# Performance work log

Hardware: AMD Instinct MI355X
Metric: run time of the kernel (lower is better)

## Reference

```python
import jax, jax.numpy as jnp
import numpy as np

INTERVAL = 8
HEADS = 4
DIM = 64


def grid_shuffle(x, I):
    # rearrange 'b c (h i) (w j) -> (b i j) c h w' : stride-I residue grouping
    B, C, H, W = x.shape
    h, w = H // I, W // I
    x = x.reshape(B, C, h, I, w, I).transpose(0, 3, 5, 1, 2, 4)
    return x.reshape(B * I * I, C, h, w)


def grid_unshuffle(x, I, B):
    Bp, C, h, w = x.shape
    x = x.reshape(B, I, I, C, h, w).transpose(0, 3, 4, 1, 5, 2)
    return x.reshape(B, C, h * I, w * I)


def conv1x1(x, w, b):
    return jnp.einsum('oc,bchw->bohw', w, x) + b[None, :, None, None]


def pos_bias(h, w, W1, b1, W2, b2):
    # dynamic RPE: MLP over normalized relative coordinates -> [heads, N, N]
    ch = jnp.arange(h)
    cw = jnp.arange(w)
    coords = jnp.stack(jnp.meshgrid(ch, cw, indexing='ij'), -1).reshape(-1, 2).astype(jnp.float32)
    denom = jnp.array([max(h - 1, 1), max(w - 1, 1)], dtype=jnp.float32)
    rel = (coords[:, None, :] - coords[None, :, :]) / denom  # [N,N,2]
    hid = jax.nn.relu(rel @ W1 + b1)
    bias = hid @ W2 + b2  # [N,N,heads]
    return bias.transpose(2, 0, 1)


def mask_attn(q2d, k2d, v2d, bias, pw, pb, heads, scale):
    Bp, C, h, w = q2d.shape
    N, d = h * w, C // heads

    def to_tok(t):  # [Bp,C,h,w] -> [Bp,heads,N,d]
        return t.reshape(Bp, heads, d, N).transpose(0, 1, 3, 2)

    q, k, v = to_tok(q2d), to_tok(k2d), to_tok(v2d)
    attn = jnp.einsum('bhnd,bhmd->bhnm', q * scale, k) + bias[None]
    attn = jax.nn.softmax(attn, axis=-1)
    out = jnp.einsum('bhnm,bhmd->bhnd', attn, v)
    out2d = out.transpose(0, 1, 3, 2).reshape(Bp, C, h, w)
    return conv1x1(out2d, pw, pb)


def setup_inputs() -> dict:
    key = jax.random.key(0)
    ks = jax.random.split(key, 14)
    pos_hidden = DIM // 4  # 16
    s = 0.02
    return {
        'x': jax.random.normal(ks[0], (2, DIM, 160, 160), jnp.float32),
        'qkv_w': jax.random.normal(ks[1], (3 * DIM, DIM), jnp.float32) * s,
        'qkv_b': jnp.zeros((3 * DIM,), jnp.float32),
        'grid_w': jax.random.normal(ks[2], (DIM, DIM), jnp.float32) * s,
        'grid_b': jnp.zeros((DIM,), jnp.float32),
        'pos_w1': jax.random.normal(ks[3], (2, pos_hidden), jnp.float32) * s,
        'pos_b1': jnp.zeros((pos_hidden,), jnp.float32),
        'pos_w2': jax.random.normal(ks[4], (pos_hidden, HEADS), jnp.float32) * s,
        'pos_b2': jnp.zeros((HEADS,), jnp.float32),
        'proj1_w': jax.random.normal(ks[5], (DIM, DIM), jnp.float32) * s,
        'proj1_b': jnp.zeros((DIM,), jnp.float32),
        'proj2_w': jax.random.normal(ks[6], (DIM, DIM), jnp.float32) * s,
        'proj2_b': jnp.zeros((DIM,), jnp.float32),
    }


def reference(x, qkv_w, qkv_b, grid_w, grid_b, pos_w1, pos_b1, pos_w2, pos_b2,
              proj1_w, proj1_b, proj2_w, proj2_b):
    I = INTERVAL
    scale = (DIM // HEADS) ** -0.5
    B, C, H, W = x.shape
    qkv = conv1x1(x, qkv_w, qkv_b)
    x_grid = conv1x1(grid_shuffle(x, I), grid_w, grid_b)
    qkv = grid_shuffle(qkv, I)
    bias = pos_bias(H // I, W // I, pos_w1, pos_b1, pos_w2, pos_b2)
    q, k, v = jnp.split(qkv, 3, axis=1)
    out = mask_attn(x_grid, k, v, bias, proj1_w, proj1_b, HEADS, scale)
    out = mask_attn(q, x_grid, out, bias, proj2_w, proj2_b, HEADS, scale)
    return grid_unshuffle(out, I, B)
```

## Files before the change

kernel.cpp:

```cpp
#include <hip/hip_runtime.h>
#include <hip/hip_bf16.h>


#define N_TOK 400
#define NP    416
#define BP    128

typedef short bf16x8 __attribute__((ext_vector_type(8)));
typedef float f32x16 __attribute__((ext_vector_type(16)));

__device__ inline ushort f2bf(float f) {
    __hip_bfloat16 h = __float2bfloat16(f);
    return *reinterpret_cast<ushort*>(&h);
}
__device__ inline float bf2f(ushort u) {
    union { uint i; float f; } v; v.i = (uint)u << 16; return v.f;
}
__device__ inline uint pk2(float a, float b) {
    return (uint)f2bf(a) | ((uint)f2bf(b) << 16);
}
__device__ inline bf16x8 ld16(const ushort* p) {
    union { uint4 q; bf16x8 v; } u;
    u.q = *reinterpret_cast<const uint4*>(p);
    return u.v;
}
__device__ inline float fast_exp2(float x) {
#if __has_builtin(__builtin_amdgcn_exp2f)
    return __builtin_amdgcn_exp2f(x);
#else
    return __expf(x * 0.6931471805599453f);
#endif
}
__device__ inline float fast_rcp(float x) {
#if __has_builtin(__builtin_amdgcn_rcpf)
    return __builtin_amdgcn_rcpf(x);
#else
    return 1.0f / x;
#endif
}

#define L2E 1.4426950408889634f
#define QK_PRESCALE 0.36067376022224085f

__global__ __launch_bounds__(256) void k_prep(
    const float* __restrict__ W1, const float* __restrict__ B1,
    const float* __restrict__ W2, const float* __restrict__ B2,
    const float* __restrict__ qkv_w, const float* __restrict__ qkv_b,
    const float* __restrict__ grid_w, const float* __restrict__ grid_b,
    const float* __restrict__ p1w, const float* __restrict__ p2w,
    float* __restrict__ biasF, ushort* __restrict__ Wc, float* __restrict__ Bc,
    ushort* __restrict__ Wp1, ushort* __restrict__ Wp2)
{
    int blk = blockIdx.x;
    if (blk < 2704) {
        int idx = blk * 256 + threadIdx.x;
        if (idx >= 692224) return;
        int r = idx & 15, lane = (idx >> 4) & 63;
        int tile = idx >> 10;
        int mt = tile % 13, rem = tile / 13, qt = rem % 13, h = rem / 13;
        int n = qt * 32 + (lane & 31);
        int m = mt * 32 + (r & 3) + 8 * (r >> 2) + 4 * (lane >> 5);
        float val = 0.0f;
        if (n < 400 && m < 400) {
            float r0 = (float)(n / 20 - m / 20) * (1.0f / 19.0f);
            float r1 = (float)(n % 20 - m % 20) * (1.0f / 19.0f);
            float o = B2[h];
#pragma unroll
            for (int k = 0; k < 16; ++k) {
                float hh = r0 * W1[k] + r1 * W1[16 + k] + B1[k];
                hh = fmaxf(hh, 0.0f);
                o += hh * W2[k * 4 + h];
            }
            val = o * L2E;
        }
        biasF[idx] = val;
    } else {
        int t = (blk - 2704) * 256 + threadIdx.x;
        if (t < 16384) {
            int oc = t >> 6, k = t & 63;
            float v = (oc < 192) ? qkv_w[oc * 64 + k] : grid_w[(oc - 192) * 64 + k];
            Wc[t] = f2bf(v);
        } else if (t < 16384 + 4096) {
            Wp1[t - 16384] = f2bf(p1w[t - 16384]);
        } else if (t < 16384 + 8192) {
            Wp2[t - 16384 - 4096] = f2bf(p2w[t - 16384 - 4096]);
        } else if (t < 16384 + 8192 + 256) {
            int oc = t - 16384 - 8192;
            Bc[oc] = (oc < 192) ? qkv_b[oc] : grid_b[oc - 192];
        }
    }
}

__global__ __launch_bounds__(256) void k_conv(
    const float* __restrict__ x, const ushort* __restrict__ Wc,
    const float* __restrict__ Bc,
    ushort* __restrict__ Qb, ushort* __restrict__ Kb,
    ushort* __restrict__ Vb, ushort* __restrict__ XGb)
{
    __shared__ __align__(16) ushort XL[32 * 64];
    int blk = blockIdx.x;
    int b = blk / 800, rem = blk % 800;
    int H0 = rem / 5, wt = rem % 5;
    int w0 = wt * 32;
    int tid = threadIdx.x;

    {
        int c = tid >> 2, q4 = tid & 3;
        const float* xr = x + ((size_t)(b * 64 + c) * 160 + H0) * 160 + w0 + q4 * 8;
        float4 f0 = *reinterpret_cast<const float4*>(xr);
        float4 f1 = *reinterpret_cast<const float4*>(xr + 4);
        char* base = reinterpret_cast<char*>(XL);
#pragma unroll
        for (int k = 0; k < 8; ++k) {
            float v = (k < 4) ? ((const float*)&f0)[k] : ((const float*)&f1)[k - 4];
            int p = q4 * 8 + k;
            int byt = p * 128 + ((2 * c) ^ ((p & 7) << 4));
            *reinterpret_cast<ushort*>(base + byt) = f2bf(v);
        }
    }

    int lane = tid & 63, w = tid >> 6;
    int l31 = lane & 31, hi = lane >> 5;

    bf16x8 wf[2][4];
#pragma unroll
    for (int nt = 0; nt < 2; ++nt)
#pragma unroll
        for (int kk = 0; kk < 4; ++kk)
            wf[nt][kk] = ld16(&Wc[(size_t)(w * 64 + nt * 32 + l31) * 64 + kk * 16 + hi * 8]);
    __syncthreads();

    f32x16 acc0 = 0.0f, acc1 = 0.0f;
    const char* base = reinterpret_cast<const char*>(XL);
#pragma unroll
    for (int kk = 0; kk < 4; ++kk) {
        int byt = l31 * 128 + (((kk * 32 + hi * 16)) ^ ((l31 & 7) << 4));
        bf16x8 xf;
        {
            union { uint4 q; bf16x8 v; } u;
            u.q = *reinterpret_cast<const uint4*>(base + byt);
            xf = u.v;
        }
        acc0 = __builtin_amdgcn_mfma_f32_32x32x16_bf16(wf[0][kk], xf, acc0, 0, 0, 0);
        acc1 = __builtin_amdgcn_mfma_f32_32x32x16_bf16(wf[1][kk], xf, acc1, 0, 0, 0);
    }

    int W0 = w0 + l31, ww = W0 >> 3, j = W0 & 7;
    int bp = b * 64 + (H0 & 7) * 8 + j;
    int n  = (H0 >> 3) * 20 + ww;
    ushort* outb = (w == 0) ? Qb : (w == 1) ? Kb : (w == 2) ? Vb : XGb;
    float mul = (w <= 1) ? QK_PRESCALE : 1.0f;
    ushort* dst = outb + ((size_t)bp * NP + n) * 64;
#pragma unroll
    for (int nt = 0; nt < 2; ++nt) {
        const f32x16& a = nt ? acc1 : acc0;
#pragma unroll
        for (int g = 0; g < 4; ++g) {
            int cc = nt * 32 + 8 * g + 4 * hi;
            int oc = w * 64 + cc;
            uint2 uu;
            uu.x = pk2((a[4 * g + 0] + Bc[oc + 0]) * mul, (a[4 * g + 1] + Bc[oc + 1]) * mul);
            uu.y = pk2((a[4 * g + 2] + Bc[oc + 2]) * mul, (a[4 * g + 3] + Bc[oc + 3]) * mul);
            *reinterpret_cast<uint2*>(dst + cc) = uu;
        }
    }
}

__global__ __launch_bounds__(512, 4) void k_attn_mfma(
    const ushort* __restrict__ Qg, const ushort* __restrict__ Kg,
    const ushort* __restrict__ Vg, const float* __restrict__ biasF,
    ushort* __restrict__ O)
{
    __shared__ ushort Ks[NP * 16];
    __shared__ ushort Vt[16 * 424];
    int blk = blockIdx.x;
    int bp = blk >> 2, h = blk & 3;
    int tid = threadIdx.x;

    const ushort* Ksrc = Kg + (size_t)bp * NP * 64 + h * 16;
#pragma unroll
    for (int it = 0; it < 2; ++it) {
        int i = tid + it * 512;
        if (i < NP * 2) {
            int row = i >> 1, half = i & 1;
            *reinterpret_cast<uint4*>(&Ks[row * 16 + half * 8]) =
                *reinterpret_cast<const uint4*>(&Ksrc[(size_t)row * 64 + half * 8]);
        }
    }
    const ushort* Vsrc = Vg + (size_t)bp * NP * 64 + h * 16;
#pragma unroll
    for (int it = 0; it < 2; ++it) {
        int i = tid + it * 512;
        if (i < 800) {
            int row = i >> 1, hf = i & 1;
            uint4 v = *reinterpret_cast<const uint4*>(&Vsrc[(size_t)row * 64 + hf * 8]);
            const ushort* pv = reinterpret_cast<const ushort*>(&v);
#pragma unroll
            for (int k = 0; k < 8; ++k)
                Vt[(hf * 8 + k) * 424 + row] = pv[k];
        }
    }
    __syncthreads();

    int lane = tid & 63, w = tid >> 6;
    int l31 = lane & 31, hi = lane >> 5;
    const uint ONE2 = 0x3F803F80u;

    for (int qt = w; qt < 13; qt += 8) {
        int qbase = qt * 32;
        bf16x8 qf = ld16(&Qg[((size_t)bp * NP + qbase + l31) * 64 + h * 16 + hi * 8]);
        f32x16 acc = 0.0f;
        const f32x16* bfr = reinterpret_cast<const f32x16*>(
            biasF + ((size_t)(h * 169 + qt * 13)) * 1024 + lane * 16);

        f32x16 cb = bfr[0];

#pragma unroll
        for (int mt = 0; mt < 13; ++mt) {
            const int mbase = mt * 32;
            f32x16 nb;
            if (mt < 12) nb = bfr[mt + 1];

            __builtin_amdgcn_s_setprio(1);
            bf16x8 kf = ld16(&Ks[(mbase + l31) * 16 + hi * 8]);
            f32x16 sv = __builtin_amdgcn_mfma_f32_32x32x16_bf16(kf, qf, cb, 0, 0, 0);

            const int nv = (mt == 12) ? 8 : 16;
            float p[16];
#pragma unroll
            for (int r = 0; r < 16; ++r)
                if (r < nv) p[r] = fast_exp2(sv[r]);

            {
                uint c4 = pk2(p[0], p[1]), c5 = pk2(p[2], p[3]);
                uint c6 = pk2(p[4], p[5]), c7 = pk2(p[6], p[7]);
                asm("v_permlane32_swap_b32 %0, %1" : "+v"(c4), "+v"(c6));
                asm("v_permlane32_swap_b32 %0, %1" : "+v"(c5), "+v"(c7));
                union { uint u[4]; bf16x8 v; } A;
                A.u[0] = c4; A.u[1] = c5; A.u[2] = c6; A.u[3] = c7;
                bf16x8 vf;
                if (l31 < 16) vf = ld16(&Vt[l31 * 424 + mbase + hi * 8]);
                else { union { uint u[4]; bf16x8 v; } o; o.u[0]=o.u[1]=o.u[2]=o.u[3]=ONE2; vf = o.v; }
                acc = __builtin_amdgcn_mfma_f32_32x32x16_bf16(A.v, vf, acc, 0, 0, 0);
            }
            if (mt < 12) {
                uint c4 = pk2(p[8], p[9]),  c5 = pk2(p[10], p[11]);
                uint c6 = pk2(p[12], p[13]), c7 = pk2(p[14], p[15]);
                asm("v_permlane32_swap_b32 %0, %1" : "+v"(c4), "+v"(c6));
                asm("v_permlane32_swap_b32 %0, %1" : "+v"(c5), "+v"(c7));
                union { uint u[4]; bf16x8 v; } A;
                A.u[0] = c4; A.u[1] = c5; A.u[2] = c6; A.u[3] = c7;
                bf16x8 vf;
                if (l31 < 16) vf = ld16(&Vt[l31 * 424 + mbase + 16 + hi * 8]);
                else { union { uint u[4]; bf16x8 v; } o; o.u[0]=o.u[1]=o.u[2]=o.u[3]=ONE2; vf = o.v; }
                acc = __builtin_amdgcn_mfma_f32_32x32x16_bf16(A.v, vf, acc, 0, 0, 0);
            }
            __builtin_amdgcn_s_setprio(0);
            cb = nb;
        }

#pragma unroll
        for (int r = 0; r < 16; ++r) {
            int moff = (r & 3) + 8 * (r >> 2) + 4 * hi;
            int q = qbase + moff;
            float s = __shfl(acc[r], lane | 16);
            if (l31 < 16 && q < N_TOK)
                O[((size_t)bp * 400 + q) * 64 + h * 16 + l31] = f2bf(acc[r] * fast_rcp(s));
        }
    }
}

template<int MODE>
__global__ __launch_bounds__(256) void k_proj(
    const ushort* __restrict__ In, const ushort* __restrict__ Wp,
    const float* __restrict__ Bv, ushort* __restrict__ Out)
{
    __shared__ __align__(16) ushort XL[128 * 64];
    size_t t0 = (size_t)blockIdx.x * 128;
    int tid = threadIdx.x;

    char* basec = reinterpret_cast<char*>(XL);
#pragma unroll
    for (int it = 0; it < 4; ++it) {
        int idx = tid + it * 256;
        int p = idx >> 3, c8 = idx & 7;
        uint4 v = *reinterpret_cast<const uint4*>(In + (t0 + p) * 64 + c8 * 8);
        int byt = p * 128 + ((c8 * 16) ^ ((p & 7) << 4));
        *reinterpret_cast<uint4*>(basec + byt) = v;
    }

    int lane = tid & 63, w = tid >> 6;
    int l31 = lane & 31, hi = lane >> 5;

    bf16x8 wf[2][4];
#pragma unroll
    for (int nt = 0; nt < 2; ++nt)
#pragma unroll
        for (int kk = 0; kk < 4; ++kk)
            wf[nt][kk] = ld16(&Wp[(size_t)(nt * 32 + l31) * 64 + kk * 16 + hi * 8]);
    __syncthreads();

    int prow = w * 32 + l31;
    f32x16 acc0 = 0.0f, acc1 = 0.0f;
#pragma unroll
    for (int kk = 0; kk < 4; ++kk) {
        int byt = prow * 128 + (((kk * 32 + hi * 16)) ^ ((prow & 7) << 4));
        union { uint4 q; bf16x8 v; } u;
        u.q = *reinterpret_cast<const uint4*>(basec + byt);
        acc0 = __builtin_amdgcn_mfma_f32_32x32x16_bf16(wf[0][kk], u.v, acc0, 0, 0, 0);
        acc1 = __builtin_amdgcn_mfma_f32_32x32x16_bf16(wf[1][kk], u.v, acc1, 0, 0, 0);
    }

    size_t t = t0 + prow;
    ushort* dst;
    if (MODE == 0) {
        int bp = (int)(t / 400), n = (int)(t % 400);
        dst = Out + ((size_t)bp * NP + n) * 64;
    } else {
        dst = Out + t * 64;
    }
#pragma unroll
    for (int nt = 0; nt < 2; ++nt) {
        const f32x16& a = nt ? acc1 : acc0;
#pragma unroll
        for (int g = 0; g < 4; ++g) {
            int cc = nt * 32 + 8 * g + 4 * hi;
            uint2 uu;
            uu.x = pk2(a[4 * g + 0] + Bv[cc + 0], a[4 * g + 1] + Bv[cc + 1]);
            uu.y = pk2(a[4 * g + 2] + Bv[cc + 2], a[4 * g + 3] + Bv[cc + 3]);
            *reinterpret_cast<uint2*>(dst + cc) = uu;
        }
    }
}

__global__ __launch_bounds__(256) void k_unshuffle(
    const ushort* __restrict__ In, float* __restrict__ out)
{
    __shared__ __align__(16) ushort il[160 * 64];
    int blk = blockIdx.x;
    int b = blk / 160, rem = blk % 160, iI = rem / 20, hh = rem % 20;
    int tid = threadIdx.x;

    for (int idx = tid; idx < 1280; idx += 256) {
        int j = idx / 160, r2 = idx % 160, ww = r2 / 8, c8 = r2 % 8;
        int bp = b * 64 + iI * 8 + j;
        int n  = hh * 20 + ww;
        uint4 v = reinterpret_cast<const uint4*>(In + ((size_t)bp * 400 + n) * 64)[c8];
        reinterpret_cast<uint4*>(&il[(ww * 8 + j) * 64])[c8] = v;
    }
    __syncthreads();

    int c = tid >> 2, q = tid & 3;
    int H0 = hh * 8 + iI;
    float* og = out + ((size_t)(b * 64 + c) * 160 + H0) * 160;
#pragma unroll
    for (int k = 0; k < 10; ++k) {
        int f = q + 4 * k;
        float4 v;
        v.x = bf2f(il[(4 * f + 0) * 64 + c]);
        v.y = bf2f(il[(4 * f + 1) * 64 + c]);
        v.z = bf2f(il[(4 * f + 2) * 64 + c]);
        v.w = bf2f(il[(4 * f + 3) * 64 + c]);
        reinterpret_cast<float4*>(og)[f] = v;
    }
}

extern "C" void kernel_launch(void* const* d_in, const int* in_sizes, int n_in,
                              void* d_out, int out_size, void* d_ws, size_t ws_size,
                              hipStream_t stream)
{
    const float* x      = (const float*)d_in[0];
    const float* qkv_w  = (const float*)d_in[1];
    const float* qkv_b  = (const float*)d_in[2];
    const float* grid_w = (const float*)d_in[3];
    const float* grid_b = (const float*)d_in[4];
    const float* pw1    = (const float*)d_in[5];
    const float* pb1    = (const float*)d_in[6];
    const float* pw2    = (const float*)d_in[7];
    const float* pb2    = (const float*)d_in[8];
    const float* p1w    = (const float*)d_in[9];
    const float* p1b    = (const float*)d_in[10];
    const float* p2w    = (const float*)d_in[11];
    const float* p2b    = (const float*)d_in[12];

    char* W = (char*)d_ws;
    float*  biasF = (float*)(W + 0);
    ushort* Wc    = (ushort*)(W + 2768896);
    ushort* Wp1   = (ushort*)(W + 2801664);
    ushort* Wp2   = (ushort*)(W + 2809856);
    float*  Bc    = (float*) (W + 2818048);
    const size_t BASE2 = 2819072;
    const size_t BB = (size_t)BP * NP * 64 * 2;
    ushort* Qb = (ushort*)(W + BASE2);
    ushort* Kb = (ushort*)(W + BASE2 + 1 * BB);
    ushort* Vb = (ushort*)(W + BASE2 + 2 * BB);
    ushort* XG = (ushort*)(W + BASE2 + 3 * BB);
    ushort* P1 = (ushort*)(W + BASE2 + 4 * BB);
    const size_t OB = (size_t)BP * 400 * 64 * 2;
    ushort* O1 = (ushort*)(W + BASE2 + 5 * BB);
    ushort* O2 = (ushort*)(W + BASE2 + 5 * BB + OB);
    ushort* OFb = O1;
    float*  out = (float*)d_out;

    k_prep<<<2801, 256, 0, stream>>>(pw1, pb1, pw2, pb2, qkv_w, qkv_b, grid_w, grid_b,
                                     p1w, p2w, biasF, Wc, Bc, Wp1, Wp2);
    k_conv<<<1600, 256, 0, stream>>>(x, Wc, Bc, Qb, Kb, Vb, XG);
    k_attn_mfma<<<512, 512, 0, stream>>>(XG, Kb, Vb, biasF, O1);
    k_proj<0><<<400, 256, 0, stream>>>(O1, Wp1, p1b, P1);
    k_attn_mfma<<<512, 512, 0, stream>>>(Qb, XG, P1, biasF, O2);
    k_proj<1><<<400, 256, 0, stream>>>(O2, Wp2, p2b, OFb);
    k_unshuffle<<<320, 256, 0, stream>>>(OFb, out);
}
```

Before: 114.8 us.

## Give each attention wave one query tile with 13-wave blocks and ones-padded V

Blocks grow from 8 waves to 13 (832 threads), so each wave handles exactly one 32-query tile instead of some waves handling two. This removes the load imbalance where 5 of 8 waves ran two tiles. The V transpose buffer in shared memory doubles, and rows 16-31 are pre-filled with bf16 ones so the per-lane branch that built the ones operand for the row-sum column goes away. Risks are fewer resident blocks per CU because of the larger block and LDS footprint, plus extra LDS fill work per block.

```diff
diff --git a/kernel.cpp b/kernel.cpp
--- a/kernel.cpp
+++ b/kernel.cpp
@@ -166,107 +166,97 @@
     }
 }
 
-__global__ __launch_bounds__(512, 4) void k_attn_mfma(
+__global__ __launch_bounds__(832) void k_attn_mfma(
     const ushort* __restrict__ Qg, const ushort* __restrict__ Kg,
     const ushort* __restrict__ Vg, const float* __restrict__ biasF,
     ushort* __restrict__ O)
 {
     __shared__ ushort Ks[NP * 16];
-    __shared__ ushort Vt[16 * 424];
+    __shared__ ushort Vt[32 * 424];
     int blk = blockIdx.x;
     int bp = blk >> 2, h = blk & 3;
     int tid = threadIdx.x;
 
-    const ushort* Ksrc = Kg + (size_t)bp * NP * 64 + h * 16;
-#pragma unroll
-    for (int it = 0; it < 2; ++it) {
-        int i = tid + it * 512;
-        if (i < NP * 2) {
-            int row = i >> 1, half = i & 1;
-            *reinterpret_cast<uint4*>(&Ks[row * 16 + half * 8]) =
-                *reinterpret_cast<const uint4*>(&Ksrc[(size_t)row * 64 + half * 8]);
-        }
-    }
-    const ushort* Vsrc = Vg + (size_t)bp * NP * 64 + h * 16;
-#pragma unroll
-    for (int it = 0; it < 2; ++it) {
-        int i = tid + it * 512;
-        if (i < 800) {
-            int row = i >> 1, hf = i & 1;
-            uint4 v = *reinterpret_cast<const uint4*>(&Vsrc[(size_t)row * 64 + hf * 8]);
-            const ushort* pv = reinterpret_cast<const ushort*>(&v);
-#pragma unroll
-            for (int k = 0; k < 8; ++k)
-                Vt[(hf * 8 + k) * 424 + row] = pv[k];
-        }
+    {
+        int row = tid >> 1, half = tid & 1;
+        const ushort* Ksrc = Kg + (size_t)bp * NP * 64 + h * 16;
+        *reinterpret_cast<uint4*>(&Ks[row * 16 + half * 8]) =
+            *reinterpret_cast<const uint4*>(&Ksrc[(size_t)row * 64 + half * 8]);
+    }
+    if (tid < 800) {
+        const ushort* Vsrc = Vg + (size_t)bp * NP * 64 + h * 16;
+        int row = tid >> 1, hf = tid & 1;
+        uint4 v = *reinterpret_cast<const uint4*>(&Vsrc[(size_t)row * 64 + hf * 8]);
+        const ushort* pv = reinterpret_cast<const ushort*>(&v);
+#pragma unroll
+        for (int k = 0; k < 8; ++k)
+            Vt[(hf * 8 + k) * 424 + row] = pv[k];
+    }
+    for (int j = tid; j < 3392; j += 832) {
+        int row = 16 + j / 212, col2 = j % 212;
+        *reinterpret_cast<uint*>(&Vt[row * 424 + col2 * 2]) = 0x3F803F80u;
     }
     __syncthreads();
 
     int lane = tid & 63, w = tid >> 6;
     int l31 = lane & 31, hi = lane >> 5;
-    const uint ONE2 = 0x3F803F80u;
-
-    for (int qt = w; qt < 13; qt += 8) {
-        int qbase = qt * 32;
-        bf16x8 qf = ld16(&Qg[((size_t)bp * NP + qbase + l31) * 64 + h * 16 + hi * 8]);
-        f32x16 acc = 0.0f;
-        const f32x16* bfr = reinterpret_cast<const f32x16*>(
-            biasF + ((size_t)(h * 169 + qt * 13)) * 1024 + lane * 16);
-
-        f32x16 cb = bfr[0];
-
-#pragma unroll
-        for (int mt = 0; mt < 13; ++mt) {
-            const int mbase = mt * 32;
-            f32x16 nb;
-            if (mt < 12) nb = bfr[mt + 1];
-
-            __builtin_amdgcn_s_setprio(1);
-            bf16x8 kf = ld16(&Ks[(mbase + l31) * 16 + hi * 8]);
-            f32x16 sv = __builtin_amdgcn_mfma_f32_32x32x16_bf16(kf, qf, cb, 0, 0, 0);
-
-            const int nv = (mt == 12) ? 8 : 16;
-            float p[16];
-#pragma unroll
-            for (int r = 0; r < 16; ++r)
-                if (r < nv) p[r] = fast_exp2(sv[r]);
-
-            {
-                uint c4 = pk2(p[0], p[1]), c5 = pk2(p[2], p[3]);
-                uint c6 = pk2(p[4], p[5]), c7 = pk2(p[6], p[7]);
-                asm("v_permlane32_swap_b32 %0, %1" : "+v"(c4), "+v"(c6));
-                asm("v_permlane32_swap_b32 %0, %1" : "+v"(c5), "+v"(c7));
-                union { uint u[4]; bf16x8 v; } A;
-                A.u[0] = c4; A.u[1] = c5; A.u[2] = c6; A.u[3] = c7;
-                bf16x8 vf;
-                if (l31 < 16) vf = ld16(&Vt[l31 * 424 + mbase + hi * 8]);
-                else { union { uint u[4]; bf16x8 v; } o; o.u[0]=o.u[1]=o.u[2]=o.u[3]=ONE2; vf = o.v; }
-                acc = __builtin_amdgcn_mfma_f32_32x32x16_bf16(A.v, vf, acc, 0, 0, 0);
-            }
-            if (mt < 12) {
-                uint c4 = pk2(p[8], p[9]),  c5 = pk2(p[10], p[11]);
-                uint c6 = pk2(p[12], p[13]), c7 = pk2(p[14], p[15]);
-                asm("v_permlane32_swap_b32 %0, %1" : "+v"(c4), "+v"(c6));
-                asm("v_permlane32_swap_b32 %0, %1" : "+v"(c5), "+v"(c7));
-                union { uint u[4]; bf16x8 v; } A;
-                A.u[0] = c4; A.u[1] = c5; A.u[2] = c6; A.u[3] = c7;
-                bf16x8 vf;
-                if (l31 < 16) vf = ld16(&Vt[l31 * 424 + mbase + 16 + hi * 8]);
-                else { union { uint u[4]; bf16x8 v; } o; o.u[0]=o.u[1]=o.u[2]=o.u[3]=ONE2; vf = o.v; }
-                acc = __builtin_amdgcn_mfma_f32_32x32x16_bf16(A.v, vf, acc, 0, 0, 0);
-            }
-            __builtin_amdgcn_s_setprio(0);
-            cb = nb;
-        }
-
-#pragma unroll
-        for (int r = 0; r < 16; ++r) {
-            int moff = (r & 3) + 8 * (r >> 2) + 4 * hi;
-            int q = qbase + moff;
-            float s = __shfl(acc[r], lane | 16);
-            if (l31 < 16 && q < N_TOK)
-                O[((size_t)bp * 400 + q) * 64 + h * 16 + l31] = f2bf(acc[r] * fast_rcp(s));
-        }
+
+    int qt = w;
+    int qbase = qt * 32;
+    bf16x8 qf = ld16(&Qg[((size_t)bp * NP + qbase + l31) * 64 + h * 16 + hi * 8]);
+    f32x16 acc = 0.0f;
+    const f32x16* bfr = reinterpret_cast<const f32x16*>(
+        biasF + ((size_t)(h * 169 + qt * 13)) * 1024 + lane * 16);
+
+    f32x16 cb = bfr[0];
+
+#pragma unroll
+    for (int mt = 0; mt < 13; ++mt) {
+        const int mbase = mt * 32;
+        f32x16 nb;
+        if (mt < 12) nb = bfr[mt + 1];
+
+        __builtin_amdgcn_s_setprio(1);
+        bf16x8 kf = ld16(&Ks[(mbase + l31) * 16 + hi * 8]);
+        f32x16 sv = __builtin_amdgcn_mfma_f32_32x32x16_bf16(kf, qf, cb, 0, 0, 0);
+
+        const int nv = (mt == 12) ? 8 : 16;
+        float p[16];
+#pragma unroll
+        for (int r = 0; r < 16; ++r)
+            if (r < nv) p[r] = fast_exp2(sv[r]);
+
+        {
+            uint c4 = pk2(p[0], p[1]), c5 = pk2(p[2], p[3]);
+            uint c6 = pk2(p[4], p[5]), c7 = pk2(p[6], p[7]);
+            asm("v_permlane32_swap_b32 %0, %1" : "+v"(c4), "+v"(c6));
+            asm("v_permlane32_swap_b32 %0, %1" : "+v"(c5), "+v"(c7));
+            union { uint u[4]; bf16x8 v; } A;
+            A.u[0] = c4; A.u[1] = c5; A.u[2] = c6; A.u[3] = c7;
+            bf16x8 vf = ld16(&Vt[l31 * 424 + mbase + hi * 8]);
+            acc = __builtin_amdgcn_mfma_f32_32x32x16_bf16(A.v, vf, acc, 0, 0, 0);
+        }
+        if (mt < 12) {
+            uint c4 = pk2(p[8], p[9]),  c5 = pk2(p[10], p[11]);
+            uint c6 = pk2(p[12], p[13]), c7 = pk2(p[14], p[15]);
+            asm("v_permlane32_swap_b32 %0, %1" : "+v"(c4), "+v"(c6));
+            asm("v_permlane32_swap_b32 %0, %1" : "+v"(c5), "+v"(c7));
+            union { uint u[4]; bf16x8 v; } A;
+            A.u[0] = c4; A.u[1] = c5; A.u[2] = c6; A.u[3] = c7;
+            bf16x8 vf = ld16(&Vt[l31 * 424 + mbase + 16 + hi * 8]);
+            acc = __builtin_amdgcn_mfma_f32_32x32x16_bf16(A.v, vf, acc, 0, 0, 0);
+        }
+        __builtin_amdgcn_s_setprio(0);
+        cb = nb;
+    }
+
+#pragma unroll
+    for (int r = 0; r < 16; ++r) {
+        int moff = (r & 3) + 8 * (r >> 2) + 4 * hi;
+        int q = qbase + moff;
+        float s = __shfl(acc[r], lane | 16);
+        if (l31 < 16 && q < N_TOK)
+            O[((size_t)bp * 400 + q) * 64 + h * 16 + l31] = f2bf(acc[r] * fast_rcp(s));
     }
 }
 
@@ -405,9 +395,9 @@
     k_prep<<<2801, 256, 0, stream>>>(pw1, pb1, pw2, pb2, qkv_w, qkv_b, grid_w, grid_b,
                                      p1w, p2w, biasF, Wc, Bc, Wp1, Wp2);
     k_conv<<<1600, 256, 0, stream>>>(x, Wc, Bc, Qb, Kb, Vb, XG);
-    k_attn_mfma<<<512, 512, 0, stream>>>(XG, Kb, Vb, biasF, O1);
+    k_attn_mfma<<<512, 832, 0, stream>>>(XG, Kb, Vb, biasF, O1);
     k_proj<0><<<400, 256, 0, stream>>>(O1, Wp1, p1b, P1);
-    k_attn_mfma<<<512, 512, 0, stream>>>(Qb, XG, P1, biasF, O2);
+    k_attn_mfma<<<512, 832, 0, stream>>>(Qb, XG, P1, biasF, O2);
     k_proj<1><<<400, 256, 0, stream>>>(O2, Wp2, p2b, OFb);
     k_unshuffle<<<320, 256, 0, stream>>>(OFb, out);
 }
```

After: 117.8 us. 2.6% more time.
